# Kernel optimization log

Measured on AMD Instinct MI355X. Metric: run time of the kernel, lower is better.

## Reference

```python
import jax, jax.numpy as jnp
import numpy as np

B, C, Himg, Wimg = 4, 256, 64, 64
HID = 256
K = 8
EPS_NORM = 1e-12
BN_EPS = 1e-5


def setup_inputs() -> dict:
    key = jax.random.key(0)
    ks = jax.random.split(key, 14)
    s = lambda fan: 1.0 / np.sqrt(fan)
    inp = {
        "features": jax.random.normal(ks[0], (B, C, Himg, Wimg), dtype=jnp.float32),
        # HypergraphConv 0: theta (C->HID), phi (HID->HID). Weights stored [in,out].
        "theta0_w": jax.random.normal(ks[1], (C, HID), dtype=jnp.float32) * s(C),
        "theta0_b": jnp.zeros((HID,), jnp.float32),
        "phi0_w": jax.random.normal(ks[2], (HID, HID), dtype=jnp.float32) * s(HID),
        "phi0_b": jnp.zeros((HID,), jnp.float32),
        # HypergraphConv 1: theta (HID->HID), phi (HID->HID)
        "theta1_w": jax.random.normal(ks[3], (HID, HID), dtype=jnp.float32) * s(HID),
        "theta1_b": jnp.zeros((HID,), jnp.float32),
        "phi1_w": jax.random.normal(ks[4], (HID, HID), dtype=jnp.float32) * s(HID),
        "phi1_b": jnp.zeros((HID,), jnp.float32),
        # out_proj: 1x1 conv HID->C, stored as [HID, C]
        "proj_w": jax.random.normal(ks[5], (HID, C), dtype=jnp.float32) * s(HID),
        "proj_b": jnp.zeros((C,), jnp.float32),
        # BatchNorm2d affine params
        "bn_gamma": jnp.ones((C,), jnp.float32),
        "bn_beta": jnp.zeros((C,), jnp.float32),
    }
    return inp


def _build_hypergraph(features):
    # features: [B, C, H, W] -> nodes [B, N, C]; incidence from batch 0 only
    b, c, h, w = features.shape
    n = h * w
    feat_flat = features.reshape(b, c, n).transpose(0, 2, 1)  # [B, N, C]
    f0 = feat_flat[0]  # [N, C] (original computes full-batch similarity but uses [0])
    f0n = f0 / jnp.maximum(jnp.linalg.norm(f0, axis=-1, keepdims=True), EPS_NORM)
    sim = f0n @ f0n.T  # [N, N]
    _, idx = jax.lax.top_k(sim, K)  # [N, K]
    rows = idx.reshape(-1)
    cols = jnp.repeat(jnp.arange(n), K)
    Hm = jnp.zeros((n, n), jnp.float32).at[rows, cols].set(1.0)  # [N, E=N]
    # L1 column normalization (F.normalize p=1 dim=0)
    Hn = Hm / jnp.maximum(Hm.sum(axis=0, keepdims=True), EPS_NORM)
    return Hn, feat_flat


def _hconv(x, Hn, tw, tb, pw, pb):
    # x: [B, N, Cin]
    xt = x @ tw + tb  # [B, N, Cout]
    ef = jnp.einsum('ne,bnc->bec', Hn, xt)  # H^T @ x_theta -> edge feats
    xp = ef @ pw + pb  # [B, E, Cout]
    return jnp.einsum('ne,bec->bnc', Hn, xp)  # H @ x_phi


def reference(features, theta0_w, theta0_b, phi0_w, phi0_b,
              theta1_w, theta1_b, phi1_w, phi1_b,
              proj_w, proj_b, bn_gamma, bn_beta):
    b, c, h, w = features.shape
    Hn, x = _build_hypergraph(features)
    x = jax.nn.relu(_hconv(x, Hn, theta0_w, theta0_b, phi0_w, phi0_b))
    x = jax.nn.relu(_hconv(x, Hn, theta1_w, theta1_b, phi1_w, phi1_b)) + x
    # back to [B, HID, H, W] then 1x1 conv
    x = x.transpose(0, 2, 1).reshape(b, HID, h, w)
    x = jnp.einsum('bihw,io->bohw', x, proj_w) + proj_b[None, :, None, None]
    # BatchNorm2d (training mode: batch statistics, biased variance)
    mean = x.mean(axis=(0, 2, 3))
    var = x.var(axis=(0, 2, 3))
    xn = (x - mean[None, :, None, None]) * jax.lax.rsqrt(var + BN_EPS)[None, :, None, None]
    xn = xn * bn_gamma[None, :, None, None] + bn_beta[None, :, None, None]
    return features + xn
```

## Files before the change

kernel.cpp:

```cpp
#include <hip/hip_runtime.h>

namespace {

constexpr int NB = 4;
constexpr int NC = 256;
constexpr int NN = 4096;

typedef __attribute__((ext_vector_type(8))) short bf8;
typedef __attribute__((ext_vector_type(4))) float f4;
typedef unsigned short ushort_t;
typedef unsigned long long ull;

__device__ __forceinline__ float bf2f(unsigned short u) {
  return __uint_as_float(((unsigned)u) << 16);
}
__device__ __forceinline__ unsigned short f2bf(float f) {
  unsigned x = __float_as_uint(f);
  return (unsigned short)((x + 0x7FFFu + ((x >> 16) & 1u)) >> 16);
}
__device__ __forceinline__ unsigned enc_f(float f) {
  unsigned u = __float_as_uint(f);
  return (u & 0x80000000u) ? ~u : (u | 0x80000000u);
}
__device__ __forceinline__ float dec_e(unsigned e) {
  return __uint_as_float((e & 0x80000000u) ? (e ^ 0x80000000u) : ~e);
}

__device__ __forceinline__ void ins8(ull* b, ull k) {
  if (k <= b[7]) return;
  b[7] = k;
#pragma unroll
  for (int p = 7; p >= 1; --p) {
    if (b[p] > b[p-1]) { ull t = b[p]; b[p] = b[p-1]; b[p-1] = t; }
  }
}

__device__ __forceinline__ ull shfl_xor_ull(ull v, int mask) {
  unsigned lo = (unsigned)(v & 0xFFFFFFFFull), hi = (unsigned)(v >> 32);
  lo = (unsigned)__shfl_xor((int)lo, mask);
  hi = (unsigned)__shfl_xor((int)hi, mask);
  return ((ull)hi << 32) | (ull)lo;
}

template<int MAXS>
__device__ __forceinline__ void shfl_merge8(ull* b) {
#pragma unroll
  for (int s = 1; s <= MAXS; s <<= 1) {
    ull tmp[8];
#pragma unroll
    for (int k = 0; k < 8; ++k) tmp[k] = shfl_xor_ull(b[k], s);
#pragma unroll
    for (int k = 0; k < 8; ++k) ins8(b, tmp[k]);
  }
}

__global__ __launch_bounds__(256) void norm_kernel(const float* __restrict__ feat,
                                                   float* __restrict__ inv,
                                                   int* __restrict__ counts,
                                                   float* __restrict__ bnsum) {
  int n = blockIdx.x * 256 + threadIdx.x;
  counts[n] = 0;
  if (n < 2 * NC) bnsum[n] = 0.f;
  float ss = 0.f;
  for (int c = 0; c < NC; ++c) { float v = feat[(size_t)c * NN + n]; ss = fmaf(v, v, ss); }
  inv[n] = 1.f / fmaxf(sqrtf(ss), 1e-12f);
}

__global__ __launch_bounds__(256) void feat2bf_kernel(const float* __restrict__ feat,
                                                      const float* __restrict__ inv,
                                                      unsigned short* __restrict__ xin,
                                                      unsigned short* __restrict__ Xhi,
                                                      unsigned short* __restrict__ Xlo) {
  __shared__ float tile[64][65];
  int n0 = blockIdx.x * 64, c0 = blockIdx.y * 64, b = blockIdx.z;
  int tid = threadIdx.x;
#pragma unroll
  for (int i = 0; i < 4; ++i) {
    int u = tid + i * 256; int cr = u >> 4, q = u & 15;
    float4 v = *(const float4*)&feat[((size_t)b * NC + c0 + cr) * NN + n0 + q * 4];
    tile[cr][q*4+0] = v.x; tile[cr][q*4+1] = v.y; tile[cr][q*4+2] = v.z; tile[cr][q*4+3] = v.w;
  }
  __syncthreads();
#pragma unroll
  for (int i = 0; i < 4; ++i) {
    int u = tid + i * 256; int nr = u >> 4, q = u & 15;
    float x0 = tile[q*4+0][nr], x1 = tile[q*4+1][nr];
    float x2 = tile[q*4+2][nr], x3 = tile[q*4+3][nr];
    ushort4 o;
    o.x = f2bf(x0); o.y = f2bf(x1); o.z = f2bf(x2); o.w = f2bf(x3);
    *(ushort4*)&xin[((size_t)(b << 12) + n0 + nr) * NC + c0 + q * 4] = o;
    if (b == 0) {
      float iv = inv[n0 + nr];
      float y0 = x0 * iv, y1 = x1 * iv, y2 = x2 * iv, y3 = x3 * iv;
      ushort4 h, l;
      h.x = f2bf(y0); l.x = f2bf(y0 - bf2f(h.x));
      h.y = f2bf(y1); l.y = f2bf(y1 - bf2f(h.y));
      h.z = f2bf(y2); l.z = f2bf(y2 - bf2f(h.z));
      h.w = f2bf(y3); l.w = f2bf(y3 - bf2f(h.w));
      size_t oo = (size_t)(n0 + nr) * NC + c0 + q * 4;
      *(ushort4*)&Xhi[oo] = h;
      *(ushort4*)&Xlo[oo] = l;
    }
  }
}

__global__ __launch_bounds__(256) void wcvt_kernel(const float* __restrict__ w0,
                                                   const float* __restrict__ w1,
                                                   const float* __restrict__ w2,
                                                   const float* __restrict__ w3,
                                                   const float* __restrict__ w4,
                                                   unsigned short* __restrict__ Wt) {
  __shared__ float tile[64][65];
  int z = blockIdx.z;
  const float* W = (z == 0) ? w0 : (z == 1) ? w1 : (z == 2) ? w2 : (z == 3) ? w3 : w4;
  int k0 = blockIdx.x * 64, n0 = blockIdx.y * 64;
  int tid = threadIdx.x;
#pragma unroll
  for (int i = 0; i < 4; ++i) {
    int u = tid + i * 256; int kr = u >> 4, q = u & 15;
    float4 v = *(const float4*)&W[(size_t)(k0 + kr) * NC + n0 + q * 4];
    tile[kr][q*4+0] = v.x; tile[kr][q*4+1] = v.y; tile[kr][q*4+2] = v.z; tile[kr][q*4+3] = v.w;
  }
  __syncthreads();
#pragma unroll
  for (int i = 0; i < 4; ++i) {
    int u = tid + i * 256; int nr = u >> 4, q = u & 15;
    ushort4 o;
    o.x = f2bf(tile[q*4+0][nr]); o.y = f2bf(tile[q*4+1][nr]);
    o.z = f2bf(tile[q*4+2][nr]); o.w = f2bf(tile[q*4+3][nr]);
    *(ushort4*)&Wt[(size_t)z * 65536 + (size_t)(n0 + nr) * NC + k0 + q * 4] = o;
  }
}

__global__ __launch_bounds__(512) void simtop_kernel(const unsigned short* __restrict__ Xhi,
                                                     const unsigned short* __restrict__ Xlo,
                                                     ull* __restrict__ cand) {
  __shared__ __align__(16) char lds[73728];
  float (*simT)[132] = (float(*)[132])(lds);

  int tid = threadIdx.x, wave = tid >> 6, lane = tid & 63;
  int wm = wave >> 2, wn = wave & 3;
  int orig = blockIdx.x;
  int bid = (orig & 7) * 66 + (orig >> 3);
  int pi = (int)((sqrtf(8.f * (float)bid + 1.f) - 1.f) * 0.5f);
  while ((pi + 1) * (pi + 2) / 2 <= bid) ++pi;
  while (pi * (pi + 1) / 2 > bid) --pi;
  int pj = bid - pi * (pi + 1) / 2;
  int m0 = pj * 128, n0 = pi * 128;

  int sr = tid >> 2;
  int q0 = (tid & 3) * 2;
  int s_ = (sr >> 1) & 7;
  int qp0 = q0 ^ s_;
  const ushort_t* gAh = Xhi + (size_t)(m0 + sr) * NC + q0 * 8;
  const ushort_t* gAl = Xlo + (size_t)(m0 + sr) * NC + q0 * 8;
  const ushort_t* gBh = Xhi + (size_t)(n0 + sr) * NC + q0 * 8;
  const ushort_t* gBl = Xlo + (size_t)(n0 + sr) * NC + q0 * 8;
  int d0 = sr * 144 + qp0 * 16;
  int d1 = sr * 144 + (qp0 ^ 1) * 16;

  int oA[2][4], oB[2][2];
#pragma unroll
  for (int ks = 0; ks < 2; ++ks) {
    int qr = ks * 4 + (lane >> 4);
#pragma unroll
    for (int mf = 0; mf < 4; ++mf) {
      int rr = wm * 64 + mf * 16 + (lane & 15);
      oA[ks][mf] = rr * 144 + (qr ^ ((rr >> 1) & 7)) * 16;
    }
#pragma unroll
    for (int nf = 0; nf < 2; ++nf) {
      int rr = wn * 32 + nf * 16 + (lane & 15);
      oB[ks][nf] = rr * 144 + (qr ^ ((rr >> 1) & 7)) * 16;
    }
  }

  f4 acc[4][2];
#pragma unroll
  for (int i = 0; i < 4; ++i)
#pragma unroll
    for (int j = 0; j < 2; ++j) acc[i][j] = (f4){0.f, 0.f, 0.f, 0.f};

#pragma unroll
  for (int kk = 0; kk < 4; ++kk) {
    {
      uint4 a0 = *(const uint4*)(gAh + kk * 64);
      uint4 a1 = *(const uint4*)(gAh + kk * 64 + 8);
      uint4 a2 = *(const uint4*)(gAl + kk * 64);
      uint4 a3 = *(const uint4*)(gAl + kk * 64 + 8);
      uint4 b0 = *(const uint4*)(gBh + kk * 64);
      uint4 b1 = *(const uint4*)(gBh + kk * 64 + 8);
      uint4 b2 = *(const uint4*)(gBl + kk * 64);
      uint4 b3 = *(const uint4*)(gBl + kk * 64 + 8);
      *(uint4*)(lds +         d0) = a0;  *(uint4*)(lds +         d1) = a1;
      *(uint4*)(lds + 18432 + d0) = a2;  *(uint4*)(lds + 18432 + d1) = a3;
      *(uint4*)(lds + 36864 + d0) = b0;  *(uint4*)(lds + 36864 + d1) = b1;
      *(uint4*)(lds + 55296 + d0) = b2;  *(uint4*)(lds + 55296 + d1) = b3;
    }
    __syncthreads();
#pragma unroll
    for (int ks = 0; ks < 2; ++ks) {
      bf8 ah[4], al[4], bh[2], bl[2];
#pragma unroll
      for (int mf = 0; mf < 4; ++mf) {
        ah[mf] = *(const bf8*)(lds +         oA[ks][mf]);
        al[mf] = *(const bf8*)(lds + 18432 + oA[ks][mf]);
      }
#pragma unroll
      for (int nf = 0; nf < 2; ++nf) {
        bh[nf] = *(const bf8*)(lds + 36864 + oB[ks][nf]);
        bl[nf] = *(const bf8*)(lds + 55296 + oB[ks][nf]);
      }
#pragma unroll
      for (int nf = 0; nf < 2; ++nf)
#pragma unroll
        for (int mf = 0; mf < 4; ++mf) {
          acc[mf][nf] = __builtin_amdgcn_mfma_f32_16x16x32_bf16(ah[mf], bh[nf], acc[mf][nf], 0, 0, 0);
          acc[mf][nf] = __builtin_amdgcn_mfma_f32_16x16x32_bf16(ah[mf], bl[nf], acc[mf][nf], 0, 0, 0);
          acc[mf][nf] = __builtin_amdgcn_mfma_f32_16x16x32_bf16(al[mf], bh[nf], acc[mf][nf], 0, 0, 0);
        }
    }
    __syncthreads();
  }

#pragma unroll
  for (int mf = 0; mf < 4; ++mf)
#pragma unroll
    for (int nf = 0; nf < 2; ++nf) {
      int cl = wn * 32 + nf * 16 + (lane & 15);
      int rbase = wm * 64 + mf * 16 + (lane >> 4) * 4;
#pragma unroll
      for (int r = 0; r < 4; ++r)
        simT[rbase + r][cl] = acc[mf][nf][r];
    }
  __syncthreads();

  {
    int rl = tid >> 2, q4 = tid & 3;
    const float* rowp = &simT[rl][q4 * 32];
    ull b8[8] = {0,0,0,0,0,0,0,0};
    float thr = -3.0e38f;
#pragma unroll
    for (int i = 0; i < 8; ++i) {
      int off = ((i + q4 * 2) & 7) * 4;
      float4 v = *(const float4*)(rowp + off);
      if (fmaxf(fmaxf(v.x, v.y), fmaxf(v.z, v.w)) >= thr) {
        int jb = n0 + q4 * 32 + off;
        ins8(b8, ((ull)enc_f(v.x) << 32) | (ull)(0xFFFFFFFFu - (unsigned)(jb + 0)));
        ins8(b8, ((ull)enc_f(v.y) << 32) | (ull)(0xFFFFFFFFu - (unsigned)(jb + 1)));
        ins8(b8, ((ull)enc_f(v.z) << 32) | (ull)(0xFFFFFFFFu - (unsigned)(jb + 2)));
        ins8(b8, ((ull)enc_f(v.w) << 32) | (ull)(0xFFFFFFFFu - (unsigned)(jb + 3)));
        unsigned h = (unsigned)(b8[7] >> 32);
        thr = h ? dec_e(h) : -3.0e38f;
      }
    }
    shfl_merge8<2>(b8);
    if (q4 == 0) {
      ull* dst = cand + (size_t)(m0 + rl) * 256 + pi * 8;
#pragma unroll
      for (int k = 0; k < 8; ++k) dst[k] = b8[k];
    }
  }

  if (pi != pj) {
    int ccol = tid >> 2, seg = tid & 3;
    ull c8[8] = {0,0,0,0,0,0,0,0};
    float thr = -3.0e38f;
    for (int i = 0; i < 32; ++i) {
      int rr = seg * 32 + ((i + seg) & 31);
      float v = simT[rr][ccol];
      if (v >= thr) {
        ins8(c8, ((ull)enc_f(v) << 32) | (ull)(0xFFFFFFFFu - (unsigned)(m0 + rr)));
        unsigned h = (unsigned)(c8[7] >> 32);
        thr = h ? dec_e(h) : -3.0e38f;
      }
    }
    shfl_merge8<2>(c8);
    if (seg == 0) {
      ull* dst = cand + (size_t)(n0 + ccol) * 256 + pj * 8;
#pragma unroll
      for (int k = 0; k < 8; ++k) dst[k] = c8[k];
    }
  }
}

__global__ __launch_bounds__(256) void merge_kernel(const ull* __restrict__ cand,
                                                    int* __restrict__ idx8,
                                                    int* __restrict__ counts) {
  int t = blockIdx.x * 256 + threadIdx.x;
  int row = t >> 3, part = t & 7;
  const ull* cp = cand + (size_t)row * 256 + part * 32;
  ull b8[8] = {0,0,0,0,0,0,0,0};
  for (int g = 0; g < 4; ++g) {
#pragma unroll 1
    for (int k = 0; k < 8; ++k) {
      ull key = cp[g * 8 + k];
      if (key <= b8[7]) break;
      ins8(b8, key);
    }
  }
  shfl_merge8<4>(b8);
  if (part == 0) {
#pragma unroll
    for (int k = 0; k < 8; ++k) {
      int j = (int)(0xFFFFFFFFu - (unsigned)(b8[k] & 0xFFFFFFFFull));
      idx8[row * 8 + k] = j;
      atomicAdd(&counts[j], 1);
    }
  }
}

__global__ __launch_bounds__(256) void scan_kernel(const int* __restrict__ counts,
                                                   int* __restrict__ offsets,
                                                   int* __restrict__ cursor) {
  __shared__ int ssum[256];
  __shared__ int sbase[257];
  int t = threadIdx.x;
  int loc[16];
  int s = 0;
#pragma unroll
  for (int i = 0; i < 16; ++i) { loc[i] = s; s += counts[t*16 + i]; }
  ssum[t] = s;
  __syncthreads();
  if (t == 0) {
    int acc = 0;
    for (int i = 0; i < 256; ++i) { sbase[i] = acc; acc += ssum[i]; }
    sbase[256] = acc;
  }
  __syncthreads();
  int b0 = sbase[t];
#pragma unroll
  for (int i = 0; i < 16; ++i) {
    int off = b0 + loc[i];
    offsets[t*16 + i] = off;
    cursor [t*16 + i] = off;
  }
  if (t == 0) offsets[NN] = sbase[256];
}

__global__ __launch_bounds__(256) void fill_kernel(const int* __restrict__ idx8,
                                                   int* __restrict__ cursor,
                                                   int* __restrict__ edgelist) {
  int t = blockIdx.x * 256 + threadIdx.x;
  int n = idx8[t];
  int pos = atomicAdd(&cursor[n], 1);
  edgelist[pos] = t >> 3;
}

template<int OUTF32, int BNS, int GATHER>
__global__ __launch_bounds__(512) void gemm_bf16_kernel(const unsigned short* __restrict__ A,
                                                        const unsigned short* __restrict__ Wt,
                                                        const float* __restrict__ bias,
                                                        void* __restrict__ outp,
                                                        float* __restrict__ bnsum,
                                                        const int* __restrict__ idx8) {
  __shared__ ushort_t sA[128][72];
  __shared__ ushort_t sB[128][72];
  __shared__ int sIdx[128][8];
  int tid = threadIdx.x, wave = tid >> 6, lane = tid & 63;
  int wm = wave >> 2, wn = wave & 3;
  int n0 = blockIdx.x * 128, m0 = blockIdx.y * 128;
  size_t bbase = 0;
  if constexpr (GATHER) {
    int e0 = m0 & 4095;
    bbase = ((size_t)(m0 >> 12) << 12) * NC;
#pragma unroll
    for (int u = tid; u < 1024; u += 512) ((int*)sIdx)[u] = idx8[e0 * 8 + u];
    __syncthreads();
  }
  f4 acc[4][2];
#pragma unroll
  for (int i = 0; i < 4; ++i)
#pragma unroll
    for (int j = 0; j < 2; ++j) acc[i][j] = (f4){0.f, 0.f, 0.f, 0.f};

  for (int k0 = 0; k0 < NC; k0 += 64) {
#pragma unroll
    for (int i = 0; i < 2; ++i) {
      int u = tid + i * 512; int r = u >> 3, q = u & 7;
      int qp = (q ^ ((r >> 1) & 7)) * 8;
      if constexpr (GATHER) {
        float s[8] = {0.f,0.f,0.f,0.f,0.f,0.f,0.f,0.f};
#pragma unroll
        for (int k = 0; k < 8; ++k) {
          int nn = sIdx[r][k];
          uint4 v = *(const uint4*)&A[bbase + (size_t)nn * NC + k0 + q * 8];
          s[0] += bf2f((unsigned short)(v.x & 0xFFFF)); s[1] += bf2f((unsigned short)(v.x >> 16));
          s[2] += bf2f((unsigned short)(v.y & 0xFFFF)); s[3] += bf2f((unsigned short)(v.y >> 16));
          s[4] += bf2f((unsigned short)(v.z & 0xFFFF)); s[5] += bf2f((unsigned short)(v.z >> 16));
          s[6] += bf2f((unsigned short)(v.w & 0xFFFF)); s[7] += bf2f((unsigned short)(v.w >> 16));
        }
        uint4 o;
        o.x = (unsigned)f2bf(s[0]*0.125f) | ((unsigned)f2bf(s[1]*0.125f) << 16);
        o.y = (unsigned)f2bf(s[2]*0.125f) | ((unsigned)f2bf(s[3]*0.125f) << 16);
        o.z = (unsigned)f2bf(s[4]*0.125f) | ((unsigned)f2bf(s[5]*0.125f) << 16);
        o.w = (unsigned)f2bf(s[6]*0.125f) | ((unsigned)f2bf(s[7]*0.125f) << 16);
        *(uint4*)&sA[r][qp] = o;
      } else {
        *(uint4*)&sA[r][qp] = *(const uint4*)&A[(size_t)(m0 + r) * NC + k0 + q * 8];
      }
      *(uint4*)&sB[r][qp] = *(const uint4*)&Wt[(size_t)(n0 + r) * NC + k0 + q * 8];
    }
    __syncthreads();
#pragma unroll
    for (int ks = 0; ks < 2; ++ks) {
      int qr = ks * 4 + (lane >> 4);
      bf8 a[4], b[2];
#pragma unroll
      for (int mf = 0; mf < 4; ++mf) {
        int rr = wm*64 + mf*16 + (lane & 15);
        a[mf] = *(const bf8*)&sA[rr][(qr ^ ((rr >> 1) & 7)) * 8];
      }
#pragma unroll
      for (int nf = 0; nf < 2; ++nf) {
        int rr = wn*32 + nf*16 + (lane & 15);
        b[nf] = *(const bf8*)&sB[rr][(qr ^ ((rr >> 1) & 7)) * 8];
      }
#pragma unroll
      for (int nf = 0; nf < 2; ++nf)
#pragma unroll
        for (int mf = 0; mf < 4; ++mf)
          acc[mf][nf] = __builtin_amdgcn_mfma_f32_16x16x32_bf16(a[mf], b[nf], acc[mf][nf], 0, 0, 0);
    }
    __syncthreads();
  }
#pragma unroll
  for (int nf = 0; nf < 2; ++nf) {
    int n = n0 + wn*32 + nf*16 + (lane & 15);
    float bi = bias[n];
    float s1 = 0.f, s2 = 0.f;
#pragma unroll
    for (int mf = 0; mf < 4; ++mf) {
#pragma unroll
      for (int r = 0; r < 4; ++r) {
        int m = m0 + wm*64 + mf*16 + (lane >> 4)*4 + r;
        float v = acc[mf][nf][r] + bi;
        if (OUTF32) ((float*)outp)[(size_t)m * NC + n] = v;
        else ((unsigned short*)outp)[(size_t)m * NC + n] = f2bf(v);
        if (BNS) { s1 += v; s2 = fmaf(v, v, s2); }
      }
    }
    if (BNS) {
      s1 += __shfl_xor(s1, 16); s1 += __shfl_xor(s1, 32);
      s2 += __shfl_xor(s2, 16); s2 += __shfl_xor(s2, 32);
      if (lane < 16) {
        atomicAdd(&bnsum[n], s1);
        atomicAdd(&bnsum[NC + n], s2);
      }
    }
  }
}

template<int MODE>
__global__ __launch_bounds__(256) void scatter_kernel(const unsigned short* __restrict__ xp,
                                                      const int* __restrict__ offsets,
                                                      const int* __restrict__ edgelist,
                                                      const unsigned short* __restrict__ res,
                                                      unsigned short* __restrict__ outb) {
  int b = blockIdx.y;
  int n = blockIdx.x * 4 + (threadIdx.x >> 6);
  int lane = threadIdx.x & 63;
  int s0i = offsets[n], s1i = offsets[n + 1];
  float s0 = 0, s1 = 0, s2 = 0, s3 = 0;
  for (int j = s0i; j < s1i; ++j) {
    int e = edgelist[j];
    uint2 v = *(const uint2*)&xp[((size_t)((b << 12) + e)) * NC + lane * 4];
    s0 += bf2f((unsigned short)(v.x & 0xFFFF)); s1 += bf2f((unsigned short)(v.x >> 16));
    s2 += bf2f((unsigned short)(v.y & 0xFFFF)); s3 += bf2f((unsigned short)(v.y >> 16));
  }
  s0 = fmaxf(s0 * 0.125f, 0.f); s1 = fmaxf(s1 * 0.125f, 0.f);
  s2 = fmaxf(s2 * 0.125f, 0.f); s3 = fmaxf(s3 * 0.125f, 0.f);
  size_t o = ((size_t)((b << 12) + n)) * NC + lane * 4;
  if (MODE == 1) {
    uint2 v = *(const uint2*)&res[o];
    s0 += bf2f((unsigned short)(v.x & 0xFFFF)); s1 += bf2f((unsigned short)(v.x >> 16));
    s2 += bf2f((unsigned short)(v.y & 0xFFFF)); s3 += bf2f((unsigned short)(v.y >> 16));
  }
  uint2 ov;
  ov.x = (unsigned)f2bf(s0) | ((unsigned)f2bf(s1) << 16);
  ov.y = (unsigned)f2bf(s2) | ((unsigned)f2bf(s3) << 16);
  *(uint2*)&outb[o] = ov;
}

__global__ __launch_bounds__(256) void final_kernel(const float* __restrict__ y,
                                                    const float* __restrict__ feat,
                                                    const float* __restrict__ bnsum,
                                                    const float* __restrict__ gam,
                                                    const float* __restrict__ bet,
                                                    float* __restrict__ out) {
  __shared__ float tile[64][65];
  __shared__ float sa_[64], sb_[64];
  int n0 = blockIdx.x * 64;
  int c0 = blockIdx.y * 64;
  int b  = blockIdx.z;
  int tid = threadIdx.x;
  if (tid < 64) {
    const float invn = 1.f / (float)(NB * NN);
    int c = c0 + tid;
    float mean = bnsum[c] * invn;
    float var  = bnsum[NC + c] * invn - mean * mean;
    float a = gam[c] * rsqrtf(var + 1e-5f);
    sa_[tid] = a;
    sb_[tid] = bet[c] - mean * a;
  }
  int n_l = tid >> 2;
  int q   = tid & 3;
  const float4* y4 = (const float4*)y;
#pragma unroll
  for (int i = 0; i < 4; ++i) {
    int cl = q * 16 + i * 4;
    float4 v = y4[(size_t)(b * NN + n0 + n_l) * 64 + ((c0 + cl) >> 2)];
    tile[n_l][cl+0] = v.x; tile[n_l][cl+1] = v.y; tile[n_l][cl+2] = v.z; tile[n_l][cl+3] = v.w;
  }
  __syncthreads();
  int cl2 = tid >> 6;
  int nl2 = tid & 63;
#pragma unroll
  for (int p = 0; p < 16; ++p) {
    int ci = p * 4 + cl2;
    float a = sa_[ci], bb = sb_[ci];
    size_t o = (size_t)b * (NC * NN) + (size_t)(c0 + ci) * NN + n0 + nl2;
    out[o] = feat[o] + fmaf(a, tile[nl2][ci], bb);
  }
}

}

extern "C" void kernel_launch(void* const* d_in, const int* in_sizes, int n_in,
                              void* d_out, int out_size, void* d_ws, size_t ws_size,
                              hipStream_t stream) {
  (void)in_sizes; (void)n_in; (void)out_size; (void)ws_size;
  const float* feat = (const float*)d_in[0];
  const float* t0w  = (const float*)d_in[1];
  const float* t0b  = (const float*)d_in[2];
  const float* p0w  = (const float*)d_in[3];
  const float* p0b  = (const float*)d_in[4];
  const float* t1w  = (const float*)d_in[5];
  const float* t1b  = (const float*)d_in[6];
  const float* p1w  = (const float*)d_in[7];
  const float* p1b  = (const float*)d_in[8];
  const float* pw   = (const float*)d_in[9];
  const float* pb   = (const float*)d_in[10];
  const float* gam  = (const float*)d_in[11];
  const float* bet  = (const float*)d_in[12];
  float* out = (float*)d_out;

  char* ws = (char*)d_ws;
  float*          y   = (float*)ws;
  unsigned short* xin = (unsigned short*)(ws + (16u << 20));
  unsigned short* xt  = (unsigned short*)(ws + (24u << 20));
  unsigned short* xp  = (unsigned short*)(ws + (40u << 20));
  unsigned short* x1  = (unsigned short*)(ws + (48u << 20));
  unsigned short* x2  = (unsigned short*)(ws + (56u << 20));
  unsigned short* Xhi = (unsigned short*)(ws + (64u << 20));
  unsigned short* Xlo = (unsigned short*)(ws + (66u << 20));
  ull*            cand = (ull*)(ws + (68u << 20));
  char* sm = ws + (76u << 20);
  unsigned short* Wt  = (unsigned short*)sm;
  int*   idx8     = (int*)(sm + 655360);
  int*   counts   = (int*)(sm + 786432);
  int*   offsets  = (int*)(sm + 802816);
  int*   cursor   = (int*)(sm + 819456);
  int*   edgelist = (int*)(sm + 835840);
  float* inv      = (float*)(sm + 966912);
  float* bnsum    = (float*)(sm + 983296);

  norm_kernel<<<NN / 256, 256, 0, stream>>>(feat, inv, counts, bnsum);
  feat2bf_kernel<<<dim3(64, 4, 4), 256, 0, stream>>>(feat, inv, xin, Xhi, Xlo);
  wcvt_kernel<<<dim3(4, 4, 5), 256, 0, stream>>>(t0w, p0w, t1w, p1w, pw, Wt);

  simtop_kernel<<<528, 512, 0, stream>>>(Xhi, Xlo, cand);
  merge_kernel<<<128, 256, 0, stream>>>(cand, idx8, counts);
  scan_kernel<<<1, 256, 0, stream>>>(counts, offsets, cursor);
  fill_kernel<<<128, 256, 0, stream>>>(idx8, cursor, edgelist);

  gemm_bf16_kernel<0,0,0><<<dim3(2, 128), 512, 0, stream>>>(xin, Wt + 0*65536, t0b, xt, nullptr, nullptr);
  gemm_bf16_kernel<0,0,1><<<dim3(2, 128), 512, 0, stream>>>(xt,  Wt + 1*65536, p0b, xp, nullptr, idx8);
  scatter_kernel<0><<<dim3(1024, 4), 256, 0, stream>>>(xp, offsets, edgelist, nullptr, x1);
  gemm_bf16_kernel<0,0,0><<<dim3(2, 128), 512, 0, stream>>>(x1, Wt + 2*65536, t1b, xt, nullptr, nullptr);
  gemm_bf16_kernel<0,0,1><<<dim3(2, 128), 512, 0, stream>>>(xt, Wt + 3*65536, p1b, xp, nullptr, idx8);
  scatter_kernel<1><<<dim3(1024, 4), 256, 0, stream>>>(xp, offsets, edgelist, x1, x2);
  gemm_bf16_kernel<1,1,0><<<dim3(2, 128), 512, 0, stream>>>(x2, Wt + 4*65536, pb, y, bnsum, nullptr);

  final_kernel<<<dim3(64, 4, 4), 256, 0, stream>>>(y, feat, bnsum, gam, bet, out);
}
```

Baseline: 342.4 us.

## Shrink simtop LDS footprint, use branchless double-keyed top-k sorting network

The similarity/top-k kernel now stages K in 32-wide slices (8 iterations) with a smaller LDS buffer and writes the sim tile in two 64-row halves, so the LDS budget drops from 72KB to 40KB and launch bounds request higher occupancy. Top-k candidate keys are packed as a 44-bit integer (value encoding plus 12-bit index) converted to double, so insertion becomes a branchless fmax/fmin network instead of conditional 64-bit swaps. Row and column top-k now run concurrently on separate thread halves. The cost is twice as many barriers in the GEMM loop, an extra barrier for the half-tile passes, and the loss of the threshold-based early skip.

```diff
diff --git a/kernel.cpp b/kernel.cpp
--- a/kernel.cpp
+++ b/kernel.cpp
@@ -22,35 +22,34 @@
   unsigned u = __float_as_uint(f);
   return (u & 0x80000000u) ? ~u : (u | 0x80000000u);
 }
-__device__ __forceinline__ float dec_e(unsigned e) {
-  return __uint_as_float((e & 0x80000000u) ? (e ^ 0x80000000u) : ~e);
-}
-
-__device__ __forceinline__ void ins8(ull* b, ull k) {
-  if (k <= b[7]) return;
-  b[7] = k;
+
+__device__ __forceinline__ void insd(double* b, double k) {
+  b[7] = fmax(b[7], k);
 #pragma unroll
   for (int p = 7; p >= 1; --p) {
-    if (b[p] > b[p-1]) { ull t = b[p]; b[p] = b[p-1]; b[p-1] = t; }
-  }
-}
-
-__device__ __forceinline__ ull shfl_xor_ull(ull v, int mask) {
-  unsigned lo = (unsigned)(v & 0xFFFFFFFFull), hi = (unsigned)(v >> 32);
-  lo = (unsigned)__shfl_xor((int)lo, mask);
-  hi = (unsigned)__shfl_xor((int)hi, mask);
-  return ((ull)hi << 32) | (ull)lo;
+    double hi = fmax(b[p-1], b[p]);
+    double lo = fmin(b[p-1], b[p]);
+    b[p-1] = hi; b[p] = lo;
+  }
+}
+
+__device__ __forceinline__ double shfl_xor_d(double v, int m) {
+  ull u = __double_as_longlong(v);
+  unsigned lo = (unsigned)(u & 0xFFFFFFFFull), hi = (unsigned)(u >> 32);
+  lo = (unsigned)__shfl_xor((int)lo, m);
+  hi = (unsigned)__shfl_xor((int)hi, m);
+  return __longlong_as_double(((ull)hi << 32) | (ull)lo);
 }
 
 template<int MAXS>
-__device__ __forceinline__ void shfl_merge8(ull* b) {
+__device__ __forceinline__ void shfl_merged(double* b) {
 #pragma unroll
   for (int s = 1; s <= MAXS; s <<= 1) {
-    ull tmp[8];
-#pragma unroll
-    for (int k = 0; k < 8; ++k) tmp[k] = shfl_xor_ull(b[k], s);
-#pragma unroll
-    for (int k = 0; k < 8; ++k) ins8(b, tmp[k]);
+    double tmp[8];
+#pragma unroll
+    for (int k = 0; k < 8; ++k) tmp[k] = shfl_xor_d(b[k], s);
+#pragma unroll
+    for (int k = 0; k < 8; ++k) insd(b, tmp[k]);
   }
 }
 
@@ -132,10 +131,10 @@
   }
 }
 
-__global__ __launch_bounds__(512) void simtop_kernel(const unsigned short* __restrict__ Xhi,
-                                                     const unsigned short* __restrict__ Xlo,
-                                                     ull* __restrict__ cand) {
-  __shared__ __align__(16) char lds[73728];
+__global__ __launch_bounds__(512, 6) void simtop_kernel(const unsigned short* __restrict__ Xhi,
+                                                        const unsigned short* __restrict__ Xlo,
+                                                        double* __restrict__ cand) {
+  __shared__ __align__(16) char lds[40960];
   float (*simT)[132] = (float(*)[132])(lds);
 
   int tid = threadIdx.x, wave = tid >> 6, lane = tid & 63;
@@ -149,31 +148,13 @@
   int m0 = pj * 128, n0 = pi * 128;
 
   int sr = tid >> 2;
-  int q0 = (tid & 3) * 2;
-  int s_ = (sr >> 1) & 7;
-  int qp0 = q0 ^ s_;
-  const ushort_t* gAh = Xhi + (size_t)(m0 + sr) * NC + q0 * 8;
-  const ushort_t* gAl = Xlo + (size_t)(m0 + sr) * NC + q0 * 8;
-  const ushort_t* gBh = Xhi + (size_t)(n0 + sr) * NC + q0 * 8;
-  const ushort_t* gBl = Xlo + (size_t)(n0 + sr) * NC + q0 * 8;
-  int d0 = sr * 144 + qp0 * 16;
-  int d1 = sr * 144 + (qp0 ^ 1) * 16;
-
-  int oA[2][4], oB[2][2];
-#pragma unroll
-  for (int ks = 0; ks < 2; ++ks) {
-    int qr = ks * 4 + (lane >> 4);
-#pragma unroll
-    for (int mf = 0; mf < 4; ++mf) {
-      int rr = wm * 64 + mf * 16 + (lane & 15);
-      oA[ks][mf] = rr * 144 + (qr ^ ((rr >> 1) & 7)) * 16;
-    }
-#pragma unroll
-    for (int nf = 0; nf < 2; ++nf) {
-      int rr = wn * 32 + nf * 16 + (lane & 15);
-      oB[ks][nf] = rr * 144 + (qr ^ ((rr >> 1) & 7)) * 16;
-    }
-  }
+  int q  = tid & 3;
+  int qp = q ^ (sr & 3);
+  const ushort_t* gAh = Xhi + (size_t)(m0 + sr) * NC + q * 8;
+  const ushort_t* gAl = Xlo + (size_t)(m0 + sr) * NC + q * 8;
+  const ushort_t* gBh = Xhi + (size_t)(n0 + sr) * NC + q * 8;
+  const ushort_t* gBl = Xlo + (size_t)(n0 + sr) * NC + q * 8;
+  int dst = sr * 80 + qp * 16;
 
   f4 acc[4][2];
 #pragma unroll
@@ -182,34 +163,32 @@
     for (int j = 0; j < 2; ++j) acc[i][j] = (f4){0.f, 0.f, 0.f, 0.f};
 
 #pragma unroll
-  for (int kk = 0; kk < 4; ++kk) {
+  for (int kk = 0; kk < 8; ++kk) {
+    uint4 a0 = *(const uint4*)(gAh + kk * 32);
+    uint4 a1 = *(const uint4*)(gAl + kk * 32);
+    uint4 b0 = *(const uint4*)(gBh + kk * 32);
+    uint4 b1 = *(const uint4*)(gBl + kk * 32);
+    *(uint4*)(lds +     0 + dst) = a0;
+    *(uint4*)(lds + 10240 + dst) = a1;
+    *(uint4*)(lds + 20480 + dst) = b0;
+    *(uint4*)(lds + 30720 + dst) = b1;
+    __syncthreads();
     {
-      uint4 a0 = *(const uint4*)(gAh + kk * 64);
-      uint4 a1 = *(const uint4*)(gAh + kk * 64 + 8);
-      uint4 a2 = *(const uint4*)(gAl + kk * 64);
-      uint4 a3 = *(const uint4*)(gAl + kk * 64 + 8);
-      uint4 b0 = *(const uint4*)(gBh + kk * 64);
-      uint4 b1 = *(const uint4*)(gBh + kk * 64 + 8);
-      uint4 b2 = *(const uint4*)(gBl + kk * 64);
-      uint4 b3 = *(const uint4*)(gBl + kk * 64 + 8);
-      *(uint4*)(lds +         d0) = a0;  *(uint4*)(lds +         d1) = a1;
-      *(uint4*)(lds + 18432 + d0) = a2;  *(uint4*)(lds + 18432 + d1) = a3;
-      *(uint4*)(lds + 36864 + d0) = b0;  *(uint4*)(lds + 36864 + d1) = b1;
-      *(uint4*)(lds + 55296 + d0) = b2;  *(uint4*)(lds + 55296 + d1) = b3;
-    }
-    __syncthreads();
-#pragma unroll
-    for (int ks = 0; ks < 2; ++ks) {
+      int qr = lane >> 4;
       bf8 ah[4], al[4], bh[2], bl[2];
 #pragma unroll
       for (int mf = 0; mf < 4; ++mf) {
-        ah[mf] = *(const bf8*)(lds +         oA[ks][mf]);
-        al[mf] = *(const bf8*)(lds + 18432 + oA[ks][mf]);
+        int rr = wm*64 + mf*16 + (lane & 15);
+        int off = rr * 80 + ((qr ^ (rr & 3)) * 16);
+        ah[mf] = *(const bf8*)(lds +     0 + off);
+        al[mf] = *(const bf8*)(lds + 10240 + off);
       }
 #pragma unroll
       for (int nf = 0; nf < 2; ++nf) {
-        bh[nf] = *(const bf8*)(lds + 36864 + oB[ks][nf]);
-        bl[nf] = *(const bf8*)(lds + 55296 + oB[ks][nf]);
+        int rr = wn*32 + nf*16 + (lane & 15);
+        int off = rr * 80 + ((qr ^ (rr & 3)) * 16);
+        bh[nf] = *(const bf8*)(lds + 20480 + off);
+        bl[nf] = *(const bf8*)(lds + 30720 + off);
       }
 #pragma unroll
       for (int nf = 0; nf < 2; ++nf)
@@ -223,87 +202,92 @@
     __syncthreads();
   }
 
-#pragma unroll
-  for (int mf = 0; mf < 4; ++mf)
-#pragma unroll
-    for (int nf = 0; nf < 2; ++nf) {
-      int cl = wn * 32 + nf * 16 + (lane & 15);
-      int rbase = wm * 64 + mf * 16 + (lane >> 4) * 4;
-#pragma unroll
-      for (int r = 0; r < 4; ++r)
-        simT[rbase + r][cl] = acc[mf][nf][r];
-    }
-  __syncthreads();
-
-  {
-    int rl = tid >> 2, q4 = tid & 3;
-    const float* rowp = &simT[rl][q4 * 32];
-    ull b8[8] = {0,0,0,0,0,0,0,0};
-    float thr = -3.0e38f;
-#pragma unroll
-    for (int i = 0; i < 8; ++i) {
-      int off = ((i + q4 * 2) & 7) * 4;
-      float4 v = *(const float4*)(rowp + off);
-      if (fmaxf(fmaxf(v.x, v.y), fmaxf(v.z, v.w)) >= thr) {
-        int jb = n0 + q4 * 32 + off;
-        ins8(b8, ((ull)enc_f(v.x) << 32) | (ull)(0xFFFFFFFFu - (unsigned)(jb + 0)));
-        ins8(b8, ((ull)enc_f(v.y) << 32) | (ull)(0xFFFFFFFFu - (unsigned)(jb + 1)));
-        ins8(b8, ((ull)enc_f(v.z) << 32) | (ull)(0xFFFFFFFFu - (unsigned)(jb + 2)));
-        ins8(b8, ((ull)enc_f(v.w) << 32) | (ull)(0xFFFFFFFFu - (unsigned)(jb + 3)));
-        unsigned h = (unsigned)(b8[7] >> 32);
-        thr = h ? dec_e(h) : -3.0e38f;
-      }
-    }
-    shfl_merge8<2>(b8);
-    if (q4 == 0) {
-      ull* dst = cand + (size_t)(m0 + rl) * 256 + pi * 8;
-#pragma unroll
-      for (int k = 0; k < 8; ++k) dst[k] = b8[k];
-    }
-  }
-
-  if (pi != pj) {
-    int ccol = tid >> 2, seg = tid & 3;
-    ull c8[8] = {0,0,0,0,0,0,0,0};
-    float thr = -3.0e38f;
-    for (int i = 0; i < 32; ++i) {
-      int rr = seg * 32 + ((i + seg) & 31);
-      float v = simT[rr][ccol];
-      if (v >= thr) {
-        ins8(c8, ((ull)enc_f(v) << 32) | (ull)(0xFFFFFFFFu - (unsigned)(m0 + rr)));
-        unsigned h = (unsigned)(c8[7] >> 32);
-        thr = h ? dec_e(h) : -3.0e38f;
-      }
-    }
-    shfl_merge8<2>(c8);
-    if (seg == 0) {
-      ull* dst = cand + (size_t)(n0 + ccol) * 256 + pj * 8;
-#pragma unroll
-      for (int k = 0; k < 8; ++k) dst[k] = c8[k];
-    }
-  }
-}
-
-__global__ __launch_bounds__(256) void merge_kernel(const ull* __restrict__ cand,
+  double c8[8];
+  int ccol = 0, cseg = 0;
+  bool docol = (pi != pj) && (tid >= 256);
+  if (docol) {
+    ccol = (tid - 256) >> 1; cseg = tid & 1;
+#pragma unroll
+    for (int k = 0; k < 8; ++k) c8[k] = 0.0;
+  }
+
+#pragma unroll
+  for (int h = 0; h < 2; ++h) {
+    if (h) __syncthreads();
+    if (wm == h) {
+#pragma unroll
+      for (int mf = 0; mf < 4; ++mf)
+#pragma unroll
+        for (int nf = 0; nf < 2; ++nf) {
+          int cl = wn*32 + nf*16 + (lane & 15);
+          int rb = mf*16 + (lane >> 4)*4;
+#pragma unroll
+          for (int r = 0; r < 4; ++r) simT[rb + r][cl] = acc[mf][nf][r];
+        }
+    }
+    __syncthreads();
+    if (tid < 256) {
+      int rl = tid >> 2, q4 = tid & 3;
+      const float* rowp = &simT[rl][q4 * 32];
+      double b8[8] = {0,0,0,0,0,0,0,0};
+#pragma unroll
+      for (int i = 0; i < 8; ++i) {
+        int off = ((i + q4 * 2) & 7) * 4;
+        float4 v = *(const float4*)(rowp + off);
+        unsigned jb = 0xFFFu - (unsigned)(n0 + q4 * 32 + off);
+        insd(b8, (double)((((ull)enc_f(v.x)) << 12) | (ull)(jb    )));
+        insd(b8, (double)((((ull)enc_f(v.y)) << 12) | (ull)(jb - 1)));
+        insd(b8, (double)((((ull)enc_f(v.z)) << 12) | (ull)(jb - 2)));
+        insd(b8, (double)((((ull)enc_f(v.w)) << 12) | (ull)(jb - 3)));
+      }
+      shfl_merged<2>(b8);
+      if (q4 == 0) {
+        double* dp = cand + (size_t)(m0 + h * 64 + rl) * 256 + pi * 8;
+#pragma unroll
+        for (int k = 0; k < 8; ++k) dp[k] = b8[k];
+      }
+    } else if (docol) {
+#pragma unroll
+      for (int i = 0; i < 32; ++i) {
+        int ir = (i + cseg * 7) & 31;
+        int rloc = cseg * 32 + ir;
+        float v = simT[rloc][ccol];
+        unsigned jb = 0xFFFu - (unsigned)(m0 + h * 64 + rloc);
+        insd(c8, (double)((((ull)enc_f(v)) << 12) | (ull)jb));
+      }
+    }
+  }
+  if (docol) {
+    shfl_merged<1>(c8);
+    if (cseg == 0) {
+      double* dp = cand + (size_t)(n0 + ccol) * 256 + pj * 8;
+#pragma unroll
+      for (int k = 0; k < 8; ++k) dp[k] = c8[k];
+    }
+  }
+}
+
+__global__ __launch_bounds__(256) void merge_kernel(const double* __restrict__ cand,
                                                     int* __restrict__ idx8,
                                                     int* __restrict__ counts) {
   int t = blockIdx.x * 256 + threadIdx.x;
   int row = t >> 3, part = t & 7;
-  const ull* cp = cand + (size_t)row * 256 + part * 32;
-  ull b8[8] = {0,0,0,0,0,0,0,0};
+  const double* cp = cand + (size_t)row * 256 + part * 32;
+  double b8[8] = {0,0,0,0,0,0,0,0};
   for (int g = 0; g < 4; ++g) {
 #pragma unroll 1
     for (int k = 0; k < 8; ++k) {
-      ull key = cp[g * 8 + k];
+      double key = cp[g * 8 + k];
       if (key <= b8[7]) break;
-      ins8(b8, key);
-    }
-  }
-  shfl_merge8<4>(b8);
+      insd(b8, key);
+    }
+  }
+  shfl_merged<4>(b8);
   if (part == 0) {
 #pragma unroll
     for (int k = 0; k < 8; ++k) {
-      int j = (int)(0xFFFFFFFFu - (unsigned)(b8[k] & 0xFFFFFFFFull));
+      ull K = (ull)b8[k];
+      int j = 0xFFF - (int)(K & 0xFFFull);
       idx8[row * 8 + k] = j;
       atomicAdd(&counts[j], 1);
     }
@@ -377,14 +361,14 @@
   for (int k0 = 0; k0 < NC; k0 += 64) {
 #pragma unroll
     for (int i = 0; i < 2; ++i) {
-      int u = tid + i * 512; int r = u >> 3, q = u & 7;
-      int qp = (q ^ ((r >> 1) & 7)) * 8;
+      int u = tid + i * 512; int r = u >> 3; int qq = u & 7;
+      int qp = (qq ^ ((r >> 1) & 7)) * 8;
       if constexpr (GATHER) {
         float s[8] = {0.f,0.f,0.f,0.f,0.f,0.f,0.f,0.f};
 #pragma unroll
         for (int k = 0; k < 8; ++k) {
           int nn = sIdx[r][k];
-          uint4 v = *(const uint4*)&A[bbase + (size_t)nn * NC + k0 + q * 8];
+          uint4 v = *(const uint4*)&A[bbase + (size_t)nn * NC + k0 + qq * 8];
           s[0] += bf2f((unsigned short)(v.x & 0xFFFF)); s[1] += bf2f((unsigned short)(v.x >> 16));
           s[2] += bf2f((unsigned short)(v.y & 0xFFFF)); s[3] += bf2f((unsigned short)(v.y >> 16));
           s[4] += bf2f((unsigned short)(v.z & 0xFFFF)); s[5] += bf2f((unsigned short)(v.z >> 16));
@@ -397,9 +381,9 @@
         o.w = (unsigned)f2bf(s[6]*0.125f) | ((unsigned)f2bf(s[7]*0.125f) << 16);
         *(uint4*)&sA[r][qp] = o;
       } else {
-        *(uint4*)&sA[r][qp] = *(const uint4*)&A[(size_t)(m0 + r) * NC + k0 + q * 8];
-      }
-      *(uint4*)&sB[r][qp] = *(const uint4*)&Wt[(size_t)(n0 + r) * NC + k0 + q * 8];
+        *(uint4*)&sA[r][qp] = *(const uint4*)&A[(size_t)(m0 + r) * NC + k0 + qq * 8];
+      }
+      *(uint4*)&sB[r][qp] = *(const uint4*)&Wt[(size_t)(n0 + r) * NC + k0 + qq * 8];
     }
     __syncthreads();
 #pragma unroll
@@ -554,7 +538,7 @@
   unsigned short* x2  = (unsigned short*)(ws + (56u << 20));
   unsigned short* Xhi = (unsigned short*)(ws + (64u << 20));
   unsigned short* Xlo = (unsigned short*)(ws + (66u << 20));
-  ull*            cand = (ull*)(ws + (68u << 20));
+  double*         cand = (double*)(ws + (68u << 20));
   char* sm = ws + (76u << 20);
   unsigned short* Wt  = (unsigned short*)sm;
   int*   idx8     = (int*)(sm + 655360);
```

Result: faster. 307.7 us (-10.1%).
